# Performance work log

Measured on AMD Instinct MI355X. Metric: run time of the kernel, lower is better.

The kernel has to match this reference:

```python
import jax, jax.numpy as jnp
import numpy as np
from jax import lax

B, T, C = 2, 2048, 1024
HEAD = 64          # head_size N
H = C // HEAD      # n_head
EPS_GN = 0.00064   # GroupNorm epsilon from module


def l2norm(x, eps=1e-12):
    inv = lax.rsqrt(jnp.sum(x * x, axis=-1, keepdims=True) + eps)
    return x * jnp.maximum(inv, eps)


def group_norm(x, gamma, beta, groups, eps):
    n, c = x.shape
    xg = x.reshape(n, groups, c // groups)
    mu = jnp.mean(xg, axis=-1, keepdims=True)
    var = jnp.mean(jnp.square(xg - mu), axis=-1, keepdims=True)
    xg = (xg - mu) * lax.rsqrt(var + eps)
    return xg.reshape(n, c) * gamma + beta


def rwkv7_scan(r, w, k, v, a, b):
    # all [B,T,H,N]; w is log-decay, actual per-channel decay = exp(-exp(w))
    decay = jnp.exp(-jnp.exp(w))

    def step(state, inp):  # state: [B,H,N,N] (value dim i, key dim j)
        r_t, d_t, k_t, v_t, a_t, b_t = inp  # each [B,H,N]
        sa = jnp.einsum('bhij,bhj->bhi', state, a_t)
        state = (state * d_t[:, :, None, :]
                 + sa[:, :, :, None] * b_t[:, :, None, :]
                 + v_t[:, :, :, None] * k_t[:, :, None, :])
        out = jnp.einsum('bhij,bhj->bhi', state, r_t)
        return state, out

    xs = tuple(jnp.moveaxis(t, 1, 0) for t in (r, decay, k, v, a, b))
    state0 = jnp.zeros((r.shape[0], H, HEAD, HEAD), r.dtype)
    final_state, out = lax.scan(step, state0, xs)
    return jnp.moveaxis(out, 0, 1), final_state


def setup_inputs():
    key = jax.random.key(0)
    ks = jax.random.split(key, 32)

    def p(i, shape, scale=0.02):
        return jax.random.normal(ks[i], shape, jnp.float32) * scale

    return dict(
        x=jax.random.normal(ks[0], (B, T, C), jnp.float32),
        v_first=jax.random.normal(ks[1], (B, T, C), jnp.float32),
        x_r=p(2, (1, 1, C)), x_w=p(3, (1, 1, C)), x_k=p(4, (1, 1, C)),
        x_v=p(5, (1, 1, C)), x_a=p(6, (1, 1, C)), x_g=p(7, (1, 1, C)),
        w0=p(8, (1, 1, C)), w1=p(9, (C, 64)), w2=p(10, (64, C)),
        a0=p(11, (1, 1, C)), a1=p(12, (C, 64)), a2=p(13, (64, C)),
        v0=p(14, (1, 1, C)), v1=p(15, (C, 32)), v2=p(16, (32, C)),
        g1=p(17, (C, 128)), g2=p(18, (128, C)),
        k_k=p(19, (1, 1, C), 0.5), k_a=p(20, (1, 1, C), 0.5),
        r_k=p(21, (H, HEAD), 0.5),
        Wr=p(22, (C, C)), Wk=p(23, (C, C)), Wv=p(24, (C, C)), Wo=p(25, (C, C)),
        ln_gamma=jnp.ones((C,), jnp.float32),
        ln_beta=jnp.zeros((C,), jnp.float32),
    )


def reference(x, v_first, x_r, x_w, x_k, x_v, x_a, x_g, w0, w1, w2,
              a0, a1, a2, v0, v1, v2, g1, g2, k_k, k_a, r_k,
              Wr, Wk, Wv, Wo, ln_gamma, ln_beta):
    # time_shift(x) - x
    xx = jnp.pad(x, ((0, 0), (1, 0), (0, 0)))[:, :-1] - x
    xr = x + xx * x_r
    xw = x + xx * x_w
    xk = x + xx * x_k
    xv = x + xx * x_v
    xa = x + xx * x_a
    xg = x + xx * x_g

    r = xr @ Wr
    k = xk @ Wk
    v = xv @ Wv
    w = -jax.nn.softplus(-(w0 + jnp.tanh(xw @ w1) @ w2)) - 0.5
    # v_first provided (non-first layer path)
    v = v + (v_first - v) * jax.nn.sigmoid(v0 + (xv @ v1) @ v2)
    a = jax.nn.sigmoid(a0 + (xa @ a1) @ a2)
    g = jax.nn.sigmoid(xg @ g1) @ g2

    kk = l2norm((k * k_k).reshape(B, T, H, HEAD)).reshape(B, T, C)
    k = k * (1.0 + (a - 1.0) * k_a)

    r4 = r.reshape(B, T, H, HEAD)
    y, _ = rwkv7_scan(r4,
                      w.reshape(B, T, H, HEAD),
                      k.reshape(B, T, H, HEAD),
                      v.reshape(B, T, H, HEAD),
                      (-kk).reshape(B, T, H, HEAD),
                      (kk * a).reshape(B, T, H, HEAD))

    y = group_norm(y.reshape(B * T, C), ln_gamma, ln_beta, H, EPS_GN).reshape(B, T, C)

    k4 = k.reshape(B, T, H, HEAD)
    v4 = v.reshape(B, T, H, HEAD)
    rwkv = jnp.sum(r4 * k4 * r_k, axis=-1, keepdims=True) * v4  # [B,T,H,N]
    y = y + rwkv.reshape(B, T, C)
    return (y * g) @ Wo
```

## Files before the change

kernel.cpp:

```cpp
#include <hip/hip_runtime.h>
#include <hip/hip_bf16.h>
#include <math.h>

#define TSEQ 2048
#define HEADS 16
#define HSZ 64
#define CDIM 1024
#define MROWS 4096
#define CHUNK 64
#define NCHUNK (TSEQ/CHUNK)
#define NBH 32
#define LSTR 68
#define K2 2048

typedef short bf16x8 __attribute__((ext_vector_type(8)));
typedef short bf16x4 __attribute__((ext_vector_type(4)));
typedef float f32x4 __attribute__((ext_vector_type(4)));

__device__ __forceinline__ float sigf(float x) { return 1.0f / (1.0f + expf(-x)); }

__device__ __forceinline__ short to_bf16(float f) {
    __hip_bfloat16 h = __float2bfloat16(f);
    return *reinterpret_cast<short*>(&h);
}

__global__ __launch_bounds__(256)
void mix_make(const float* __restrict__ x, short* __restrict__ ax)
{
    const int m = blockIdx.x;
    const int cc = threadIdx.x * 4;
    const float4 xv = *(const float4*)(x + (size_t)m*CDIM + cc);
    float4 xp = make_float4(0.f, 0.f, 0.f, 0.f);
    if ((m & (TSEQ-1)) != 0) xp = *(const float4*)(x + (size_t)(m-1)*CDIM + cc);
    bf16x4 a, b;
    a[0] = to_bf16(xv.x); a[1] = to_bf16(xv.y);
    a[2] = to_bf16(xv.z); a[3] = to_bf16(xv.w);
    b[0] = to_bf16(xp.x - xv.x); b[1] = to_bf16(xp.y - xv.y);
    b[2] = to_bf16(xp.z - xv.z); b[3] = to_bf16(xp.w - xv.w);
    *(bf16x4*)(ax + (size_t)m*K2 + cc)        = a;
    *(bf16x4*)(ax + (size_t)m*K2 + CDIM + cc) = b;
}

__global__ __launch_bounds__(256)
void transpose_cvt(const float* __restrict__ W, short* __restrict__ Wt,
                   const int K, const int N)
{
    __shared__ float t[32][33];
    const int k0 = blockIdx.y * 32, n0 = blockIdx.x * 32;
    const int lx = threadIdx.x & 31, ly = threadIdx.x >> 5;
#pragma unroll
    for (int i = 0; i < 4; ++i)
        t[ly + i*8][lx] = W[(size_t)(k0 + ly + i*8)*N + n0 + lx];
    __syncthreads();
#pragma unroll
    for (int i = 0; i < 4; ++i)
        Wt[(size_t)(n0 + ly + i*8)*K + k0 + lx] = to_bf16(t[lx][ly + i*8]);
}

__global__ __launch_bounds__(256)
void transpose_cvt_scaled(const float* __restrict__ W, const float* __restrict__ mix,
                          short* __restrict__ Wt, const int N)
{
    __shared__ float t[32][33];
    const int k0 = blockIdx.y * 32, n0 = blockIdx.x * 32;
    const int lx = threadIdx.x & 31, ly = threadIdx.x >> 5;
#pragma unroll
    for (int i = 0; i < 4; ++i)
        t[ly + i*8][lx] = W[(size_t)(k0 + ly + i*8)*N + n0 + lx];
    __syncthreads();
    const float mv = mix[k0 + lx];
#pragma unroll
    for (int i = 0; i < 4; ++i) {
        const float w = t[lx][ly + i*8];
        short* base = Wt + (size_t)(n0 + ly + i*8)*K2 + k0 + lx;
        base[0]    = to_bf16(w);
        base[CDIM] = to_bf16(mv * w);
    }
}

template<int BN, int MODE>
__global__ __launch_bounds__(256)
void gemm_mfma(const short* __restrict__ A, const short* __restrict__ Bt,
               void* __restrict__ Cptr, const int M, const int N, const int K)
{
    constexpr int BM = 128, BK = 32;
    constexpr int ASTR = BK + 8;
    constexpr int NWC = (BN >= 128) ? 2 : 1;
    constexpr int NWR = 4 / NWC;
    constexpr int WM = BM / NWR;
    constexpr int WN = BN / NWC;
    constexpr int AM = WM / 16;
    constexpr int AN = WN / 16;

    __shared__ short As[BM * ASTR];
    __shared__ short Bs[BN * ASTR];

    const int tid  = threadIdx.x;
    const int bm   = blockIdx.y * BM;
    const int bn   = blockIdx.x * BN;
    const int wid  = tid >> 6;
    const int lane = tid & 63;
    const int wr   = wid / NWC;
    const int wc   = wid % NWC;
    const int lrow = lane & 15;
    const int koff = (lane >> 4) * 8;

    f32x4 acc[AM][AN];
#pragma unroll
    for (int m = 0; m < AM; ++m)
#pragma unroll
        for (int n = 0; n < AN; ++n)
            acc[m][n] = (f32x4){0.f, 0.f, 0.f, 0.f};

    for (int k0 = 0; k0 < K; k0 += BK) {
        __syncthreads();
#pragma unroll
        for (int p = 0; p < (BM*BK)/(256*8); ++p) {
            const int c = p*256 + tid;
            const int row = c >> 2;
            const int kc  = (c & 3) * 8;
            *(bf16x8*)&As[row*ASTR + kc] =
                *(const bf16x8*)(A + (size_t)(bm+row)*K + k0 + kc);
        }
        {
            constexpr int CHUNKS = (BN*BK)/8;
#pragma unroll
            for (int p = 0; p < (CHUNKS + 255)/256; ++p) {
                const int c = p*256 + tid;
                if ((CHUNKS & 255) == 0 || c < CHUNKS) {
                    const int col = c >> 2;
                    const int kc  = (c & 3) * 8;
                    *(bf16x8*)&Bs[col*ASTR + kc] =
                        *(const bf16x8*)(Bt + (size_t)(bn+col)*K + k0 + kc);
                }
            }
        }
        __syncthreads();

        bf16x8 af[AM], bfv[AN];
#pragma unroll
        for (int m = 0; m < AM; ++m)
            af[m] = *(const bf16x8*)&As[(wr*WM + m*16 + lrow)*ASTR + koff];
#pragma unroll
        for (int n = 0; n < AN; ++n)
            bfv[n] = *(const bf16x8*)&Bs[(wc*WN + n*16 + lrow)*ASTR + koff];
#pragma unroll
        for (int m = 0; m < AM; ++m)
#pragma unroll
            for (int n = 0; n < AN; ++n)
                acc[m][n] = __builtin_amdgcn_mfma_f32_16x16x32_bf16(
                    af[m], bfv[n], acc[m][n], 0, 0, 0);
    }

    const int r0 = (lane >> 4) * 4;
#pragma unroll
    for (int m = 0; m < AM; ++m) {
#pragma unroll
        for (int n = 0; n < AN; ++n) {
#pragma unroll
            for (int j = 0; j < 4; ++j) {
                const int row = bm + wr*WM + m*16 + r0 + j;
                const int col = bn + wc*WN + n*16 + lrow;
                float vv = acc[m][n][j];
                if (MODE == 0) {
                    ((float*)Cptr)[(size_t)row*N + col] = vv;
                } else if (MODE == 1) {
                    ((float*)Cptr)[(size_t)(col >> 10)*((size_t)MROWS*CDIM)
                                   + (size_t)row*CDIM + (col & 1023)] = vv;
                } else {
                    short* o = (short*)Cptr;
                    if (bn < 64)
                        o[(size_t)row*64 + col] = to_bf16(tanhf(vv));
                    else if (bn < 96)
                        (o + (size_t)MROWS*64)[(size_t)row*32 + col - 64] = to_bf16(vv);
                    else if (bn < 160)
                        (o + (size_t)MROWS*96)[(size_t)row*64 + col - 96] = to_bf16(vv);
                    else
                        (o + (size_t)MROWS*160)[(size_t)row*128 + col - 160] = to_bf16(sigf(vv));
                }
            }
        }
    }
}

__global__ __launch_bounds__(256)
void post_kernel(const float* __restrict__ tw, const float* __restrict__ vv,
                 const float* __restrict__ aa,
                 const float* __restrict__ w0, const float* __restrict__ v0p,
                 const float* __restrict__ a0p,
                 const float* __restrict__ k_k, const float* __restrict__ k_a,
                 const float* __restrict__ vfirst,
                 float* __restrict__ kio, float* __restrict__ vio,
                 float* __restrict__ dout, float* __restrict__ kkout,
                 float* __restrict__ bout)
{
    const int m  = blockIdx.x;
    const int c4 = threadIdx.x;
    const size_t o4 = (size_t)m*256 + c4;
    const int cc = c4*4;

    const float4 twv = ((const float4*)tw)[o4];
    const float4 vvv = ((const float4*)vv)[o4];
    const float4 aav = ((const float4*)aa)[o4];
    const float4 kv  = ((const float4*)kio)[o4];
    const float4 vv0 = ((const float4*)vio)[o4];
    const float4 vfv = ((const float4*)vfirst)[o4];
    const float4 w0v = *(const float4*)(w0 + cc);
    const float4 v0v = *(const float4*)(v0p + cc);
    const float4 a0v = *(const float4*)(a0p + cc);
    const float4 kkc = *(const float4*)(k_k + cc);
    const float4 kac = *(const float4*)(k_a + cc);

    float dec[4], vnew[4], av[4], kkr[4], knew[4];
    const float tws[4] = {twv.x, twv.y, twv.z, twv.w};
    const float vvs[4] = {vvv.x, vvv.y, vvv.z, vvv.w};
    const float aas[4] = {aav.x, aav.y, aav.z, aav.w};
    const float ks[4]  = {kv.x, kv.y, kv.z, kv.w};
    const float vs[4]  = {vv0.x, vv0.y, vv0.z, vv0.w};
    const float vfs[4] = {vfv.x, vfv.y, vfv.z, vfv.w};
    const float w0s[4] = {w0v.x, w0v.y, w0v.z, w0v.w};
    const float v0s[4] = {v0v.x, v0v.y, v0v.z, v0v.w};
    const float a0s[4] = {a0v.x, a0v.y, a0v.z, a0v.w};
    const float kks[4] = {kkc.x, kkc.y, kkc.z, kkc.w};
    const float kas[4] = {kac.x, kac.y, kac.z, kac.w};

    float ss = 0.f;
#pragma unroll
    for (int i = 0; i < 4; ++i) {
        dec[i]  = expf(-0.6065306597126334f * sigf(w0s[i] + tws[i]));
        const float sv = sigf(v0s[i] + vvs[i]);
        vnew[i] = vs[i] + (vfs[i] - vs[i]) * sv;
        av[i]   = sigf(a0s[i] + aas[i]);
        kkr[i]  = ks[i] * kks[i];
        knew[i] = ks[i] * (1.f + (av[i] - 1.f) * kas[i]);
        ss = fmaf(kkr[i], kkr[i], ss);
    }
#pragma unroll
    for (int mask = 1; mask < 16; mask <<= 1) ss += __shfl_xor(ss, mask);
    const float inv = fmaxf(rsqrtf(ss + 1e-12f), 1e-12f);

    float4 decv, vnv, knv, kkv4, bv4;
    decv.x = dec[0]; decv.y = dec[1]; decv.z = dec[2]; decv.w = dec[3];
    vnv.x = vnew[0]; vnv.y = vnew[1]; vnv.z = vnew[2]; vnv.w = vnew[3];
    knv.x = knew[0]; knv.y = knew[1]; knv.z = knew[2]; knv.w = knew[3];
    kkv4.x = kkr[0]*inv; kkv4.y = kkr[1]*inv; kkv4.z = kkr[2]*inv; kkv4.w = kkr[3]*inv;
    bv4.x = kkv4.x*av[0]; bv4.y = kkv4.y*av[1]; bv4.z = kkv4.z*av[2]; bv4.w = kkv4.w*av[3];

    ((float4*)dout)[o4]  = decv;
    ((float4*)vio)[o4]   = vnv;
    ((float4*)kio)[o4]   = knv;
    ((float4*)kkout)[o4] = kkv4;
    ((float4*)bout)[o4]  = bv4;
}

__global__ __launch_bounds__(128)
void scan_pass1(const float* __restrict__ d, const float* __restrict__ k,
                const float* __restrict__ v, const float* __restrict__ kk,
                const float* __restrict__ bb,
                float* __restrict__ Gbuf, float* __restrict__ Hbuf)
{
    const int chunk = blockIdx.x;
    const int bh = blockIdx.y;
    const int b = bh >> 4, h = bh & 15;
    const int tid = threadIdx.x;
    const int lane = tid & 63;
    const int isH = tid >> 6;

    __shared__ float sv[4][64];

    float row[HSZ];
#pragma unroll
    for (int j = 0; j < HSZ; ++j)
        row[j] = (!isH && j == lane) ? 1.f : 0.f;

    size_t off = ((size_t)b*TSEQ + (size_t)chunk*CHUNK) * CDIM + h*HSZ;
    for (int t = 0; t < CHUNK; ++t, off += CDIM) {
        const float vi = isH ? v[off + lane] : 0.f;
        __syncthreads();
        if (!isH) { sv[0][lane] = kk[off + lane]; sv[2][lane] = bb[off + lane]; }
        else      { sv[1][lane] = d[off + lane];  sv[3][lane] = k[off + lane]; }
        __syncthreads();

        float g0 = 0.f, g1 = 0.f, g2 = 0.f, g3 = 0.f;
#pragma unroll
        for (int j4 = 0; j4 < 16; ++j4) {
            const float4 kv = *(const float4*)&sv[0][j4*4];
            g0 = fmaf(row[j4*4+0], kv.x, g0);
            g1 = fmaf(row[j4*4+1], kv.y, g1);
            g2 = fmaf(row[j4*4+2], kv.z, g2);
            g3 = fmaf(row[j4*4+3], kv.w, g3);
        }
        const float ga = -((g0 + g1) + (g2 + g3));

        if (isH) {
#pragma unroll
            for (int j4 = 0; j4 < 16; ++j4) {
                const float4 dv = *(const float4*)&sv[1][j4*4];
                const float4 bv = *(const float4*)&sv[2][j4*4];
                const float4 kv = *(const float4*)&sv[3][j4*4];
                row[j4*4+0] = fmaf(row[j4*4+0], dv.x, fmaf(ga, bv.x, vi * kv.x));
                row[j4*4+1] = fmaf(row[j4*4+1], dv.y, fmaf(ga, bv.y, vi * kv.y));
                row[j4*4+2] = fmaf(row[j4*4+2], dv.z, fmaf(ga, bv.z, vi * kv.z));
                row[j4*4+3] = fmaf(row[j4*4+3], dv.w, fmaf(ga, bv.w, vi * kv.w));
            }
        } else {
#pragma unroll
            for (int j4 = 0; j4 < 16; ++j4) {
                const float4 dv = *(const float4*)&sv[1][j4*4];
                const float4 bv = *(const float4*)&sv[2][j4*4];
                row[j4*4+0] = fmaf(row[j4*4+0], dv.x, ga * bv.x);
                row[j4*4+1] = fmaf(row[j4*4+1], dv.y, ga * bv.y);
                row[j4*4+2] = fmaf(row[j4*4+2], dv.z, ga * bv.z);
                row[j4*4+3] = fmaf(row[j4*4+3], dv.w, ga * bv.w);
            }
        }
    }

    float* dst = (isH ? Hbuf : Gbuf) + (((size_t)bh*NCHUNK + chunk)*HSZ + lane)*HSZ;
#pragma unroll
    for (int j4 = 0; j4 < 16; ++j4)
        *(float4*)&dst[j4*4] = make_float4(row[j4*4+0], row[j4*4+1], row[j4*4+2], row[j4*4+3]);
}

__global__ __launch_bounds__(256)
void scan_pass2(const float* __restrict__ Gbuf, const float* __restrict__ Hbuf,
                float* __restrict__ S0buf)
{
    const int rg = blockIdx.x;
    const int bh = blockIdx.y;
    const int tid = threadIdx.x;
    const int il = tid & 15;
    const int q4 = tid >> 4;
    const int row = rg*16 + il;

    __shared__ float Gs[64][68];
    __shared__ float Ssh[16][68];

    float frag[4] = {0.f, 0.f, 0.f, 0.f};
    *(float4*)&Ssh[il][q4*4] = make_float4(0.f, 0.f, 0.f, 0.f);

    for (int c = 0; c < NCHUNK; ++c) {
        const size_t mbase = ((size_t)bh*NCHUNK + c)*HSZ*HSZ;
#pragma unroll
        for (int p = 0; p < 4; ++p) {
            const int f = tid*16 + p*4;
            const int rr = f >> 6, cc = f & 63;
            *(float4*)&Gs[rr][cc] = *(const float4*)(Gbuf + mbase + f);
        }
        *(float4*)(S0buf + mbase + (size_t)row*HSZ + q4*4) =
            make_float4(frag[0], frag[1], frag[2], frag[3]);
        __syncthreads();

        float4 hv = *(const float4*)(Hbuf + mbase + (size_t)row*HSZ + q4*4);
        float a0 = hv.x, a1 = hv.y, a2 = hv.z, a3 = hv.w;
#pragma unroll
        for (int j = 0; j < 64; ++j) {
            const float sj = Ssh[il][j];
            const float4 gv = *(const float4*)&Gs[j][q4*4];
            a0 = fmaf(sj, gv.x, a0);
            a1 = fmaf(sj, gv.y, a1);
            a2 = fmaf(sj, gv.z, a2);
            a3 = fmaf(sj, gv.w, a3);
        }
        __syncthreads();
        frag[0] = a0; frag[1] = a1; frag[2] = a2; frag[3] = a3;
        *(float4*)&Ssh[il][q4*4] = make_float4(a0, a1, a2, a3);
    }
}

__device__ __forceinline__ void zero44(f32x4 a[4][4]) {
#pragma unroll
    for (int m = 0; m < 4; ++m)
#pragma unroll
        for (int n = 0; n < 4; ++n) a[m][n] = (f32x4){0.f, 0.f, 0.f, 0.f};
}

__device__ __forceinline__ void mm_nt_lds(const short* __restrict__ Ab,
                                          const short* __restrict__ Bb,
                                          f32x4 acc[4][4], const int lane)
{
    const int lrow = lane & 15;
    const int ko   = (lane >> 4) * 8;
#pragma unroll
    for (int kh = 0; kh < 2; ++kh) {
        bf16x8 af[4], bfv[4];
#pragma unroll
        for (int m = 0; m < 4; ++m)
            af[m] = *(const bf16x8*)&Ab[(m*16 + lrow)*LSTR + kh*32 + ko];
#pragma unroll
        for (int n = 0; n < 4; ++n)
            bfv[n] = *(const bf16x8*)&Bb[(n*16 + lrow)*LSTR + kh*32 + ko];
#pragma unroll
        for (int m = 0; m < 4; ++m)
#pragma unroll
            for (int n = 0; n < 4; ++n)
                acc[m][n] = __builtin_amdgcn_mfma_f32_16x16x32_bf16(
                    af[m], bfv[n], acc[m][n], 0, 0, 0);
    }
}

__device__ __forceinline__ void mm_nt_gf32(const short* __restrict__ Ab,
                                           const float* __restrict__ Bg,
                                           f32x4 acc[4][4], const int lane)
{
    const int lrow = lane & 15;
    const int ko   = (lane >> 4) * 8;
#pragma unroll
    for (int kh = 0; kh < 2; ++kh) {
        bf16x8 af[4], bfv[4];
#pragma unroll
        for (int m = 0; m < 4; ++m)
            af[m] = *(const bf16x8*)&Ab[(m*16 + lrow)*LSTR + kh*32 + ko];
#pragma unroll
        for (int n = 0; n < 4; ++n) {
            const float* p = Bg + (size_t)(n*16 + lrow)*64 + kh*32 + ko;
            const float4 u0 = *(const float4*)p;
            const float4 u1 = *(const float4*)(p + 4);
            bf16x8 bv;
            bv[0] = to_bf16(u0.x); bv[1] = to_bf16(u0.y);
            bv[2] = to_bf16(u0.z); bv[3] = to_bf16(u0.w);
            bv[4] = to_bf16(u1.x); bv[5] = to_bf16(u1.y);
            bv[6] = to_bf16(u1.z); bv[7] = to_bf16(u1.w);
            bfv[n] = bv;
        }
#pragma unroll
        for (int m = 0; m < 4; ++m)
#pragma unroll
            for (int n = 0; n < 4; ++n)
                acc[m][n] = __builtin_amdgcn_mfma_f32_16x16x32_bf16(
                    af[m], bfv[n], acc[m][n], 0, 0, 0);
    }
}

template<int MASK, bool WRN, bool WRT>
__device__ __forceinline__ void acc_store(const f32x4 acc[4][4],
                                          short* __restrict__ dst,
                                          short* __restrict__ dstT,
                                          const int lane)
{
    const int r0 = (lane >> 4) * 4;
    const int c0 = lane & 15;
#pragma unroll
    for (int m = 0; m < 4; ++m)
#pragma unroll
        for (int n = 0; n < 4; ++n)
#pragma unroll
            for (int j = 0; j < 4; ++j) {
                const int row = m*16 + r0 + j;
                const int col = n*16 + c0;
                float vv = acc[m][n][j];
                if (MASK == 1 && col >= row) vv = 0.f;
                if (MASK == 2 && col >  row) vv = 0.f;
                const short bv = to_bf16(vv);
                if (WRN) dst [row*LSTR + col] = bv;
                if (WRT) dstT[col*LSTR + row] = bv;
            }
}

__global__ __launch_bounds__(64)
void scan_pass3_mfma(const float* __restrict__ r, const float* __restrict__ d,
                     const float* __restrict__ k, const float* __restrict__ v,
                     const float* __restrict__ kk, const float* __restrict__ bb,
                     const float* __restrict__ S0buf, float* __restrict__ y)
{
    __shared__ short Ah[64*LSTR], Bh[64*LSTR], Kh[64*LSTR], Rh[64*LSTR];
    __shared__ short Vt[64*LSTR], Cb[64*LSTR], Nb[64*LSTR], Nt[64*LSTR], Xt[64*LSTR];

    const int chunk = blockIdx.x;
    const int bh = blockIdx.y;
    const int b = bh >> 4, h = bh & 15;
    const int lane = threadIdx.x;

    size_t off = ((size_t)b*TSEQ + (size_t)chunk*CHUNK)*CDIM + h*HSZ + lane;
    float run = 0.f;
    for (int t = 0; t < CHUNK; ++t, off += CDIM) {
        const float de    = d[off];
        const float cprev = run;
        run += logf(de);
        Ah[t*LSTR + lane] = to_bf16(-kk[off] * expf(cprev));
        Bh[t*LSTR + lane] = to_bf16(bb[off] * expf(-run));
        Kh[t*LSTR + lane] = to_bf16(k[off]  * expf(-run));
        Rh[t*LSTR + lane] = to_bf16(r[off]  * expf(run));
        Vt[lane*LSTR + t] = to_bf16(v[off]);
    }
    __syncthreads();

    const float* S0g = S0buf + ((size_t)bh*NCHUNK + chunk)*HSZ*HSZ;

    f32x4 acc[4][4], xacc[4][4];

    zero44(acc);  mm_nt_lds(Ah, Bh, acc, lane);
    acc_store<1, true, true>(acc, Nb, Nt, lane);
    zero44(acc);  mm_nt_lds(Ah, Kh, acc, lane);
    acc_store<1, true, false>(acc, Cb, nullptr, lane);
    __syncthreads();

    zero44(xacc);
    mm_nt_gf32(Ah, S0g, xacc, lane);
    mm_nt_lds(Cb, Vt, xacc, lane);
    acc_store<0, false, true>(xacc, nullptr, Xt, lane);
    __syncthreads();

#pragma unroll 1
    for (int rd = 0; rd < 6; ++rd) {
        mm_nt_lds(Nb, Xt, xacc, lane);
        if (rd < 5) { zero44(acc); mm_nt_lds(Nb, Nt, acc, lane); }
        __syncthreads();
        acc_store<0, false, true>(xacc, nullptr, Xt, lane);
        if (rd < 5) acc_store<0, true, true>(acc, Nb, Nt, lane);
        __syncthreads();
    }

    zero44(acc);  mm_nt_lds(Rh, Bh, acc, lane);
    acc_store<2, true, false>(acc, Cb, nullptr, lane);
    zero44(acc);  mm_nt_lds(Rh, Kh, acc, lane);
    acc_store<2, true, false>(acc, Nb, nullptr, lane);
    __syncthreads();

    zero44(acc);
    mm_nt_gf32(Rh, S0g, acc, lane);
    mm_nt_lds(Cb, Xt, acc, lane);
    mm_nt_lds(Nb, Vt, acc, lane);

    const int r0 = (lane >> 4) * 4;
    const int c0 = lane & 15;
    float* yb = y + ((size_t)b*TSEQ + (size_t)chunk*CHUNK)*CDIM + h*HSZ;
#pragma unroll
    for (int m = 0; m < 4; ++m)
#pragma unroll
        for (int n = 0; n < 4; ++n)
#pragma unroll
            for (int j = 0; j < 4; ++j)
                yb[(size_t)(m*16 + r0 + j)*CDIM + n*16 + c0] = acc[m][n][j];
}

__global__ __launch_bounds__(1024)
void gn_kernel(const float* __restrict__ r, const float* __restrict__ k,
               const float* __restrict__ v, const float* __restrict__ g,
               const float* __restrict__ rk, const float* __restrict__ gamma,
               const float* __restrict__ beta, const float* __restrict__ y,
               short* __restrict__ ybf)
{
    const int m = blockIdx.x;
    const int c = threadIdx.x;
    const size_t o = (size_t)m*CDIM + c;
    const float yv = y[o];
    float s1 = yv, s2 = yv*yv;
#pragma unroll
    for (int mask = 1; mask < 64; mask <<= 1) {
        s1 += __shfl_xor(s1, mask);
        s2 += __shfl_xor(s2, mask);
    }
    const float mu  = s1 * (1.f/HSZ);
    const float var = s2 * (1.f/HSZ) - mu*mu;
    const float gn  = (yv - mu) * rsqrtf(var + 0.00064f) * gamma[c] + beta[c];

    float p = r[o] * k[o] * rk[c];
#pragma unroll
    for (int mask = 1; mask < 64; mask <<= 1) p += __shfl_xor(p, mask);

    ybf[o] = to_bf16((gn + p * v[o]) * g[o]);
}

extern "C" void kernel_launch(void* const* d_in, const int* in_sizes, int n_in,
                              void* d_out, int out_size, void* d_ws, size_t ws_size,
                              hipStream_t stream)
{
    const float* x      = (const float*)d_in[0];
    const float* vfirst = (const float*)d_in[1];
    const float* x_r = (const float*)d_in[2];
    const float* x_w = (const float*)d_in[3];
    const float* x_k = (const float*)d_in[4];
    const float* x_v = (const float*)d_in[5];
    const float* x_a = (const float*)d_in[6];
    const float* x_g = (const float*)d_in[7];
    const float* w0  = (const float*)d_in[8];
    const float* w1  = (const float*)d_in[9];
    const float* w2  = (const float*)d_in[10];
    const float* a0  = (const float*)d_in[11];
    const float* a1  = (const float*)d_in[12];
    const float* a2  = (const float*)d_in[13];
    const float* v0p = (const float*)d_in[14];
    const float* v1  = (const float*)d_in[15];
    const float* v2  = (const float*)d_in[16];
    const float* g1  = (const float*)d_in[17];
    const float* g2  = (const float*)d_in[18];
    const float* k_k = (const float*)d_in[19];
    const float* k_a = (const float*)d_in[20];
    const float* r_k = (const float*)d_in[21];
    const float* Wr  = (const float*)d_in[22];
    const float* Wk  = (const float*)d_in[23];
    const float* Wv  = (const float*)d_in[24];
    const float* Wo  = (const float*)d_in[25];
    const float* lng = (const float*)d_in[26];
    const float* lnb = (const float*)d_in[27];
    float* outp = (float*)d_out;

    float* ws = (float*)d_ws;
    const size_t BIG = (size_t)MROWS * CDIM;
    float* rbuf  = ws + 0*BIG;
    float* kbuf  = ws + 1*BIG;
    float* vbuf  = ws + 2*BIG;
    float* dbuf  = ws + 3*BIG;
    float* kkbuf = ws + 4*BIG;
    float* bbuf  = ws + 5*BIG;
    float* gbuf  = ws + 6*BIG;
    float* ybuf  = ws + 7*BIG;
    float* smbuf = ws + 8*BIG;
    short* hwbf  = (short*)smbuf;
    short* wT    = (short*)(smbuf + (size_t)MROWS*160/2);
    short* Brkv = wT;
    short* Bsm  = Brkv + (size_t)3072*K2;
    short* WoT  = Bsm  + (size_t)288*K2;
    short* g2T  = WoT  + (size_t)CDIM*CDIM;
    short* w2T  = g2T  + (size_t)CDIM*128;
    short* v2T  = w2T  + (size_t)CDIM*64;
    short* a2T  = v2T  + (size_t)CDIM*32;
    short* axbf = a2T  + (size_t)CDIM*64;

    float* twbuf = ybuf;
    float* vvbuf = gbuf;
    float* aabuf = outp;

    float* Gbuf  = ybuf;
    float* Hbuf  = gbuf;
    float* S0buf = outp;
    short* ybf   = (short*)dbuf;
    short* ghbf  = hwbf + (size_t)MROWS*160;

    const dim3 blk(256);

    mix_make<<<dim3(MROWS), blk, 0, stream>>>(x, axbf);
    transpose_cvt_scaled<<<dim3(CDIM/32, CDIM/32), blk, 0, stream>>>(Wr, x_r, Brkv, CDIM);
    transpose_cvt_scaled<<<dim3(CDIM/32, CDIM/32), blk, 0, stream>>>(Wk, x_k, Brkv + (size_t)1024*K2, CDIM);
    transpose_cvt_scaled<<<dim3(CDIM/32, CDIM/32), blk, 0, stream>>>(Wv, x_v, Brkv + (size_t)2048*K2, CDIM);
    transpose_cvt_scaled<<<dim3(64/32,   CDIM/32), blk, 0, stream>>>(w1, x_w, Bsm, 64);
    transpose_cvt_scaled<<<dim3(32/32,   CDIM/32), blk, 0, stream>>>(v1, x_v, Bsm + (size_t)64*K2, 32);
    transpose_cvt_scaled<<<dim3(64/32,   CDIM/32), blk, 0, stream>>>(a1, x_a, Bsm + (size_t)96*K2, 64);
    transpose_cvt_scaled<<<dim3(128/32,  CDIM/32), blk, 0, stream>>>(g1, x_g, Bsm + (size_t)160*K2, 128);
    transpose_cvt<<<dim3(CDIM/32, CDIM/32), blk, 0, stream>>>(Wo, WoT, CDIM, CDIM);
    transpose_cvt<<<dim3(CDIM/32, 128/32),  blk, 0, stream>>>(g2, g2T, 128, CDIM);
    transpose_cvt<<<dim3(CDIM/32, 64/32),   blk, 0, stream>>>(w2, w2T, 64, CDIM);
    transpose_cvt<<<dim3(CDIM/32, 32/32),   blk, 0, stream>>>(v2, v2T, 32, CDIM);
    transpose_cvt<<<dim3(CDIM/32, 64/32),   blk, 0, stream>>>(a2, a2T, 64, CDIM);

    gemm_mfma<128,1><<<dim3(3072/128, MROWS/128), blk, 0, stream>>>(
        axbf, Brkv, rbuf, MROWS, 3072, K2);
    gemm_mfma<32,2><<<dim3(288/32, MROWS/128), blk, 0, stream>>>(
        axbf, Bsm, hwbf, MROWS, 288, K2);
    gemm_mfma<128,0><<<dim3(CDIM/128, MROWS/128), blk, 0, stream>>>(
        hwbf, w2T, twbuf, MROWS, CDIM, 64);
    gemm_mfma<128,0><<<dim3(CDIM/128, MROWS/128), blk, 0, stream>>>(
        hwbf + (size_t)MROWS*64, v2T, vvbuf, MROWS, CDIM, 32);
    gemm_mfma<128,0><<<dim3(CDIM/128, MROWS/128), blk, 0, stream>>>(
        hwbf + (size_t)MROWS*96, a2T, aabuf, MROWS, CDIM, 64);

    post_kernel<<<dim3(MROWS), blk, 0, stream>>>(
        twbuf, vvbuf, aabuf, w0, v0p, a0, k_k, k_a, vfirst,
        kbuf, vbuf, dbuf, kkbuf, bbuf);

    scan_pass1<<<dim3(NCHUNK, NBH), dim3(128), 0, stream>>>(
        dbuf, kbuf, vbuf, kkbuf, bbuf, Gbuf, Hbuf);
    scan_pass2<<<dim3(4, NBH), dim3(256), 0, stream>>>(Gbuf, Hbuf, S0buf);
    scan_pass3_mfma<<<dim3(NCHUNK, NBH), dim3(64), 0, stream>>>(
        rbuf, dbuf, kbuf, vbuf, kkbuf, bbuf, S0buf, ybuf);

    gemm_mfma<128,0><<<dim3(CDIM/128, MROWS/128), blk, 0, stream>>>(
        ghbf, g2T, gbuf, MROWS, CDIM, 128);

    gn_kernel<<<dim3(MROWS), dim3(1024), 0, stream>>>(
        rbuf, kbuf, vbuf, gbuf, r_k, lng, lnb, ybuf, ybf);

    gemm_mfma<128,0><<<dim3(CDIM/128, MROWS/128), blk, 0, stream>>>(
        ybf, WoT, outp, MROWS, CDIM, CDIM);
}
```

Measured before the change: 492.6 us.

## Replace sequential chunk-transition scan with WY-form MFMA pass and lighter output pass

The per-chunk transition matrices G and H are now built with MFMA matrix products in a WY-style factorisation, using the inverted triangular system from the doubling iterations. The old pass built them with a 64-step sequential recurrence on scalar FMAs. The WY factors Y and U are stored in bf16 so the third pass skips recomputing the triangular inverse and only applies them with the carried-in state. Both chunk kernels now use four waves per block, each owning 16 rows, instead of one or two waves. This adds bf16 rounding in G/H and the stored factors and reuses the axbf buffer as scratch, which may hurt accuracy.

```diff
diff --git a/kernel.cpp b/kernel.cpp
--- a/kernel.cpp
+++ b/kernel.cpp
@@ -22,6 +22,10 @@
 __device__ __forceinline__ short to_bf16(float f) {
     __hip_bfloat16 h = __float2bfloat16(f);
     return *reinterpret_cast<short*>(&h);
+}
+__device__ __forceinline__ float bf2f(short s) {
+    unsigned int u = ((unsigned int)(unsigned short)s) << 16;
+    return __uint_as_float(u);
 }
 
 __global__ __launch_bounds__(256)
@@ -253,164 +257,39 @@
     ((float4*)bout)[o4]  = bv4;
 }
 
-__global__ __launch_bounds__(128)
-void scan_pass1(const float* __restrict__ d, const float* __restrict__ k,
-                const float* __restrict__ v, const float* __restrict__ kk,
-                const float* __restrict__ bb,
-                float* __restrict__ Gbuf, float* __restrict__ Hbuf)
-{
-    const int chunk = blockIdx.x;
-    const int bh = blockIdx.y;
-    const int b = bh >> 4, h = bh & 15;
-    const int tid = threadIdx.x;
-    const int lane = tid & 63;
-    const int isH = tid >> 6;
-
-    __shared__ float sv[4][64];
-
-    float row[HSZ];
-#pragma unroll
-    for (int j = 0; j < HSZ; ++j)
-        row[j] = (!isH && j == lane) ? 1.f : 0.f;
-
-    size_t off = ((size_t)b*TSEQ + (size_t)chunk*CHUNK) * CDIM + h*HSZ;
-    for (int t = 0; t < CHUNK; ++t, off += CDIM) {
-        const float vi = isH ? v[off + lane] : 0.f;
-        __syncthreads();
-        if (!isH) { sv[0][lane] = kk[off + lane]; sv[2][lane] = bb[off + lane]; }
-        else      { sv[1][lane] = d[off + lane];  sv[3][lane] = k[off + lane]; }
-        __syncthreads();
-
-        float g0 = 0.f, g1 = 0.f, g2 = 0.f, g3 = 0.f;
-#pragma unroll
-        for (int j4 = 0; j4 < 16; ++j4) {
-            const float4 kv = *(const float4*)&sv[0][j4*4];
-            g0 = fmaf(row[j4*4+0], kv.x, g0);
-            g1 = fmaf(row[j4*4+1], kv.y, g1);
-            g2 = fmaf(row[j4*4+2], kv.z, g2);
-            g3 = fmaf(row[j4*4+3], kv.w, g3);
-        }
-        const float ga = -((g0 + g1) + (g2 + g3));
-
-        if (isH) {
-#pragma unroll
-            for (int j4 = 0; j4 < 16; ++j4) {
-                const float4 dv = *(const float4*)&sv[1][j4*4];
-                const float4 bv = *(const float4*)&sv[2][j4*4];
-                const float4 kv = *(const float4*)&sv[3][j4*4];
-                row[j4*4+0] = fmaf(row[j4*4+0], dv.x, fmaf(ga, bv.x, vi * kv.x));
-                row[j4*4+1] = fmaf(row[j4*4+1], dv.y, fmaf(ga, bv.y, vi * kv.y));
-                row[j4*4+2] = fmaf(row[j4*4+2], dv.z, fmaf(ga, bv.z, vi * kv.z));
-                row[j4*4+3] = fmaf(row[j4*4+3], dv.w, fmaf(ga, bv.w, vi * kv.w));
-            }
-        } else {
-#pragma unroll
-            for (int j4 = 0; j4 < 16; ++j4) {
-                const float4 dv = *(const float4*)&sv[1][j4*4];
-                const float4 bv = *(const float4*)&sv[2][j4*4];
-                row[j4*4+0] = fmaf(row[j4*4+0], dv.x, ga * bv.x);
-                row[j4*4+1] = fmaf(row[j4*4+1], dv.y, ga * bv.y);
-                row[j4*4+2] = fmaf(row[j4*4+2], dv.z, ga * bv.z);
-                row[j4*4+3] = fmaf(row[j4*4+3], dv.w, ga * bv.w);
-            }
-        }
-    }
-
-    float* dst = (isH ? Hbuf : Gbuf) + (((size_t)bh*NCHUNK + chunk)*HSZ + lane)*HSZ;
-#pragma unroll
-    for (int j4 = 0; j4 < 16; ++j4)
-        *(float4*)&dst[j4*4] = make_float4(row[j4*4+0], row[j4*4+1], row[j4*4+2], row[j4*4+3]);
-}
-
-__global__ __launch_bounds__(256)
-void scan_pass2(const float* __restrict__ Gbuf, const float* __restrict__ Hbuf,
-                float* __restrict__ S0buf)
-{
-    const int rg = blockIdx.x;
-    const int bh = blockIdx.y;
-    const int tid = threadIdx.x;
-    const int il = tid & 15;
-    const int q4 = tid >> 4;
-    const int row = rg*16 + il;
-
-    __shared__ float Gs[64][68];
-    __shared__ float Ssh[16][68];
-
-    float frag[4] = {0.f, 0.f, 0.f, 0.f};
-    *(float4*)&Ssh[il][q4*4] = make_float4(0.f, 0.f, 0.f, 0.f);
-
-    for (int c = 0; c < NCHUNK; ++c) {
-        const size_t mbase = ((size_t)bh*NCHUNK + c)*HSZ*HSZ;
-#pragma unroll
-        for (int p = 0; p < 4; ++p) {
-            const int f = tid*16 + p*4;
-            const int rr = f >> 6, cc = f & 63;
-            *(float4*)&Gs[rr][cc] = *(const float4*)(Gbuf + mbase + f);
-        }
-        *(float4*)(S0buf + mbase + (size_t)row*HSZ + q4*4) =
-            make_float4(frag[0], frag[1], frag[2], frag[3]);
-        __syncthreads();
-
-        float4 hv = *(const float4*)(Hbuf + mbase + (size_t)row*HSZ + q4*4);
-        float a0 = hv.x, a1 = hv.y, a2 = hv.z, a3 = hv.w;
-#pragma unroll
-        for (int j = 0; j < 64; ++j) {
-            const float sj = Ssh[il][j];
-            const float4 gv = *(const float4*)&Gs[j][q4*4];
-            a0 = fmaf(sj, gv.x, a0);
-            a1 = fmaf(sj, gv.y, a1);
-            a2 = fmaf(sj, gv.z, a2);
-            a3 = fmaf(sj, gv.w, a3);
-        }
-        __syncthreads();
-        frag[0] = a0; frag[1] = a1; frag[2] = a2; frag[3] = a3;
-        *(float4*)&Ssh[il][q4*4] = make_float4(a0, a1, a2, a3);
-    }
-}
-
-__device__ __forceinline__ void zero44(f32x4 a[4][4]) {
-#pragma unroll
-    for (int m = 0; m < 4; ++m)
-#pragma unroll
-        for (int n = 0; n < 4; ++n) a[m][n] = (f32x4){0.f, 0.f, 0.f, 0.f};
-}
-
-__device__ __forceinline__ void mm_nt_lds(const short* __restrict__ Ab,
-                                          const short* __restrict__ Bb,
-                                          f32x4 acc[4][4], const int lane)
+__device__ __forceinline__ void zero4(f32x4 a[4]) {
+#pragma unroll
+    for (int n = 0; n < 4; ++n) a[n] = (f32x4){0.f, 0.f, 0.f, 0.f};
+}
+
+__device__ __forceinline__ void mm_nt_w(const short* __restrict__ Ab,
+                                        const short* __restrict__ Bb,
+                                        f32x4 acc[4], const int lane, const int woff)
 {
     const int lrow = lane & 15;
     const int ko   = (lane >> 4) * 8;
 #pragma unroll
     for (int kh = 0; kh < 2; ++kh) {
-        bf16x8 af[4], bfv[4];
-#pragma unroll
-        for (int m = 0; m < 4; ++m)
-            af[m] = *(const bf16x8*)&Ab[(m*16 + lrow)*LSTR + kh*32 + ko];
+        const bf16x8 af = *(const bf16x8*)&Ab[(woff + lrow)*LSTR + kh*32 + ko];
+        bf16x8 bv[4];
 #pragma unroll
         for (int n = 0; n < 4; ++n)
-            bfv[n] = *(const bf16x8*)&Bb[(n*16 + lrow)*LSTR + kh*32 + ko];
-#pragma unroll
-        for (int m = 0; m < 4; ++m)
-#pragma unroll
-            for (int n = 0; n < 4; ++n)
-                acc[m][n] = __builtin_amdgcn_mfma_f32_16x16x32_bf16(
-                    af[m], bfv[n], acc[m][n], 0, 0, 0);
-    }
-}
-
-__device__ __forceinline__ void mm_nt_gf32(const short* __restrict__ Ab,
-                                           const float* __restrict__ Bg,
-                                           f32x4 acc[4][4], const int lane)
+            bv[n] = *(const bf16x8*)&Bb[(n*16 + lrow)*LSTR + kh*32 + ko];
+#pragma unroll
+        for (int n = 0; n < 4; ++n)
+            acc[n] = __builtin_amdgcn_mfma_f32_16x16x32_bf16(af, bv[n], acc[n], 0, 0, 0);
+    }
+}
+
+__device__ __forceinline__ void mm_nt_gf32_w(const short* __restrict__ Ab,
+                                             const float* __restrict__ Bg,
+                                             f32x4 acc[4], const int lane, const int woff)
 {
     const int lrow = lane & 15;
     const int ko   = (lane >> 4) * 8;
 #pragma unroll
     for (int kh = 0; kh < 2; ++kh) {
-        bf16x8 af[4], bfv[4];
-#pragma unroll
-        for (int m = 0; m < 4; ++m)
-            af[m] = *(const bf16x8*)&Ab[(m*16 + lrow)*LSTR + kh*32 + ko];
+        const bf16x8 af = *(const bf16x8*)&Ab[(woff + lrow)*LSTR + kh*32 + ko];
 #pragma unroll
         for (int n = 0; n < 4; ++n) {
             const float* p = Bg + (size_t)(n*16 + lrow)*64 + kh*32 + ko;
@@ -421,117 +300,316 @@
             bv[2] = to_bf16(u0.z); bv[3] = to_bf16(u0.w);
             bv[4] = to_bf16(u1.x); bv[5] = to_bf16(u1.y);
             bv[6] = to_bf16(u1.z); bv[7] = to_bf16(u1.w);
-            bfv[n] = bv;
-        }
-#pragma unroll
-        for (int m = 0; m < 4; ++m)
-#pragma unroll
-            for (int n = 0; n < 4; ++n)
-                acc[m][n] = __builtin_amdgcn_mfma_f32_16x16x32_bf16(
-                    af[m], bfv[n], acc[m][n], 0, 0, 0);
+            acc[n] = __builtin_amdgcn_mfma_f32_16x16x32_bf16(af, bv, acc[n], 0, 0, 0);
+        }
     }
 }
 
 template<int MASK, bool WRN, bool WRT>
-__device__ __forceinline__ void acc_store(const f32x4 acc[4][4],
-                                          short* __restrict__ dst,
-                                          short* __restrict__ dstT,
-                                          const int lane)
+__device__ __forceinline__ void acc_store_w(const f32x4 acc[4],
+                                            short* __restrict__ dst,
+                                            short* __restrict__ dstT,
+                                            const int lane, const int woff)
 {
     const int r0 = (lane >> 4) * 4;
     const int c0 = lane & 15;
 #pragma unroll
-    for (int m = 0; m < 4; ++m)
-#pragma unroll
-        for (int n = 0; n < 4; ++n)
-#pragma unroll
-            for (int j = 0; j < 4; ++j) {
-                const int row = m*16 + r0 + j;
-                const int col = n*16 + c0;
-                float vv = acc[m][n][j];
-                if (MASK == 1 && col >= row) vv = 0.f;
-                if (MASK == 2 && col >  row) vv = 0.f;
-                const short bv = to_bf16(vv);
-                if (WRN) dst [row*LSTR + col] = bv;
-                if (WRT) dstT[col*LSTR + row] = bv;
-            }
-}
-
-__global__ __launch_bounds__(64)
-void scan_pass3_mfma(const float* __restrict__ r, const float* __restrict__ d,
-                     const float* __restrict__ k, const float* __restrict__ v,
-                     const float* __restrict__ kk, const float* __restrict__ bb,
-                     const float* __restrict__ S0buf, float* __restrict__ y)
-{
-    __shared__ short Ah[64*LSTR], Bh[64*LSTR], Kh[64*LSTR], Rh[64*LSTR];
-    __shared__ short Vt[64*LSTR], Cb[64*LSTR], Nb[64*LSTR], Nt[64*LSTR], Xt[64*LSTR];
+    for (int n = 0; n < 4; ++n)
+#pragma unroll
+        for (int j = 0; j < 4; ++j) {
+            const int row = woff + r0 + j;
+            const int col = n*16 + c0;
+            float vv = acc[n][j];
+            if (MASK == 1 && col >= row) vv = 0.f;
+            if (MASK == 2 && col >  row) vv = 0.f;
+            const short bv = to_bf16(vv);
+            if (WRN) dst [row*LSTR + col] = bv;
+            if (WRT) dstT[col*LSTR + row] = bv;
+        }
+}
+
+__device__ __forceinline__ void acc_init_lds_w(f32x4 acc[4],
+                                               const short* __restrict__ src,
+                                               const int lane, const int woff)
+{
+    const int r0 = (lane >> 4) * 4;
+    const int c0 = lane & 15;
+#pragma unroll
+    for (int n = 0; n < 4; ++n)
+#pragma unroll
+        for (int j = 0; j < 4; ++j)
+            acc[n][j] = bf2f(src[(woff + r0 + j)*LSTR + n*16 + c0]);
+}
+
+__device__ __forceinline__ void acc_init_glb_w(f32x4 acc[4],
+                                               const short* __restrict__ src,
+                                               const int lane, const int woff)
+{
+    const int r0 = (lane >> 4) * 4;
+    const int c0 = lane & 15;
+#pragma unroll
+    for (int n = 0; n < 4; ++n)
+#pragma unroll
+        for (int j = 0; j < 4; ++j)
+            acc[n][j] = bf2f(src[(woff + r0 + j)*64 + n*16 + c0]);
+}
+
+__global__ __launch_bounds__(256)
+void scan_pass1_wy(const float* __restrict__ d, const float* __restrict__ k,
+                   const float* __restrict__ v, const float* __restrict__ kk,
+                   const float* __restrict__ bb,
+                   float* __restrict__ Gbuf, float* __restrict__ Hbuf,
+                   short* __restrict__ Yg, short* __restrict__ Ug)
+{
+    __shared__ short L[8*64*LSTR];
+    __shared__ float wsum[4][64];
+    __shared__ float cTl[64];
+    short* A_  = L + 0*64*LSTR;
+    short* B_  = L + 1*64*LSTR;
+    short* K_  = L + 2*64*LSTR;
+    short* V_  = L + 3*64*LSTR;
+    short* BT_ = L + 4*64*LSTR;
+    short* KT_ = L + 5*64*LSTR;
+    short* N_  = L + 6*64*LSTR;
+    short* NT_ = L + 7*64*LSTR;
 
     const int chunk = blockIdx.x;
     const int bh = blockIdx.y;
     const int b = bh >> 4, h = bh & 15;
-    const int lane = threadIdx.x;
-
-    size_t off = ((size_t)b*TSEQ + (size_t)chunk*CHUNK)*CDIM + h*HSZ + lane;
-    float run = 0.f;
-    for (int t = 0; t < CHUNK; ++t, off += CDIM) {
-        const float de    = d[off];
-        const float cprev = run;
-        run += logf(de);
-        Ah[t*LSTR + lane] = to_bf16(-kk[off] * expf(cprev));
-        Bh[t*LSTR + lane] = to_bf16(bb[off] * expf(-run));
-        Kh[t*LSTR + lane] = to_bf16(k[off]  * expf(-run));
-        Rh[t*LSTR + lane] = to_bf16(r[off]  * expf(run));
-        Vt[lane*LSTR + t] = to_bf16(v[off]);
-    }
-    __syncthreads();
-
-    const float* S0g = S0buf + ((size_t)bh*NCHUNK + chunk)*HSZ*HSZ;
-
-    f32x4 acc[4][4], xacc[4][4];
-
-    zero44(acc);  mm_nt_lds(Ah, Bh, acc, lane);
-    acc_store<1, true, true>(acc, Nb, Nt, lane);
-    zero44(acc);  mm_nt_lds(Ah, Kh, acc, lane);
-    acc_store<1, true, false>(acc, Cb, nullptr, lane);
-    __syncthreads();
-
-    zero44(xacc);
-    mm_nt_gf32(Ah, S0g, xacc, lane);
-    mm_nt_lds(Cb, Vt, xacc, lane);
-    acc_store<0, false, true>(xacc, nullptr, Xt, lane);
+    const int tid = threadIdx.x;
+    const int w = tid >> 6;
+    const int lane = tid & 63;
+    const int woff = w * 16;
+
+    const size_t base = ((size_t)b*TSEQ + (size_t)chunk*CHUNK + woff)*CDIM + h*HSZ + lane;
+    float lc[16];
+    float s = 0.f;
+#pragma unroll
+    for (int t = 0; t < 16; ++t) { s += logf(d[base + (size_t)t*CDIM]); lc[t] = s; }
+    wsum[w][lane] = s;
+    __syncthreads();
+    float pre = 0.f;
+#pragma unroll
+    for (int w2 = 0; w2 < 3; ++w2) if (w2 < w) pre += wsum[w2][lane];
+    if (w == 3) cTl[lane] = expf(pre + s);
+
+#pragma unroll
+    for (int t = 0; t < 16; ++t) {
+        const int tg = woff + t;
+        const size_t off = base + (size_t)t*CDIM;
+        const float run   = pre + lc[t];
+        const float cprev = (t == 0) ? pre : (pre + lc[t-1]);
+        const float ern   = expf(-run);
+        A_[tg*LSTR + lane] = to_bf16(-kk[off] * expf(cprev));
+        const short bv = to_bf16(bb[off] * ern);
+        B_[tg*LSTR + lane] = bv;  BT_[lane*LSTR + tg] = bv;
+        const short kv = to_bf16(k[off] * ern);
+        K_[tg*LSTR + lane] = kv;  KT_[lane*LSTR + tg] = kv;
+        V_[lane*LSTR + tg] = to_bf16(v[off]);
+    }
+    __syncthreads();
+
+    f32x4 xj[4], xi[4], tmp[4];
+
+    zero4(tmp);  mm_nt_w(A_, B_, tmp, lane, woff);
+    acc_init_lds_w(xj, A_, lane, woff);
+    acc_store_w<1, true, true>(tmp, N_, NT_, lane, woff);
+    __syncthreads();
+
+    acc_store_w<0, false, true>(xj, nullptr, B_, lane, woff);
+    zero4(tmp);  mm_nt_w(A_, K_, tmp, lane, woff);
+    __syncthreads();
+    acc_store_w<1, true, false>(tmp, K_, nullptr, lane, woff);
+    __syncthreads();
+
+    zero4(xi);  mm_nt_w(K_, V_, xi, lane, woff);
+    acc_store_w<0, false, true>(xi, nullptr, A_, lane, woff);
     __syncthreads();
 
 #pragma unroll 1
     for (int rd = 0; rd < 6; ++rd) {
-        mm_nt_lds(Nb, Xt, xacc, lane);
-        if (rd < 5) { zero44(acc); mm_nt_lds(Nb, Nt, acc, lane); }
+        mm_nt_w(N_, B_, xj, lane, woff);
+        mm_nt_w(N_, A_, xi, lane, woff);
+        if (rd < 5) { zero4(tmp); mm_nt_w(N_, NT_, tmp, lane, woff); }
         __syncthreads();
-        acc_store<0, false, true>(xacc, nullptr, Xt, lane);
-        if (rd < 5) acc_store<0, true, true>(acc, Nb, Nt, lane);
+        acc_store_w<0, false, true>(xj, nullptr, B_, lane, woff);
+        acc_store_w<0, false, true>(xi, nullptr, A_, lane, woff);
+        if (rd < 5) acc_store_w<0, true, true>(tmp, N_, NT_, lane, woff);
         __syncthreads();
     }
 
-    zero44(acc);  mm_nt_lds(Rh, Bh, acc, lane);
-    acc_store<2, true, false>(acc, Cb, nullptr, lane);
-    zero44(acc);  mm_nt_lds(Rh, Kh, acc, lane);
-    acc_store<2, true, false>(acc, Nb, nullptr, lane);
-    __syncthreads();
-
-    zero44(acc);
-    mm_nt_gf32(Rh, S0g, acc, lane);
-    mm_nt_lds(Cb, Xt, acc, lane);
-    mm_nt_lds(Nb, Vt, acc, lane);
+    const size_t mb = ((size_t)bh*NCHUNK + chunk)*HSZ*HSZ;
+    const int r0 = (lane >> 4) * 4;
+    const int c0 = lane & 15;
+
+#pragma unroll
+    for (int n = 0; n < 4; ++n)
+#pragma unroll
+        for (int j = 0; j < 4; ++j) {
+            const int row = woff + r0 + j;
+            const int col = n*16 + c0;
+            Yg[mb + row*64 + col] = to_bf16(xj[n][j]);
+            Ug[mb + row*64 + col] = to_bf16(xi[n][j]);
+        }
+
+    float ctv[4];
+#pragma unroll
+    for (int n = 0; n < 4; ++n) ctv[n] = cTl[n*16 + c0];
+
+    zero4(tmp);  mm_nt_w(B_, BT_, tmp, lane, woff);
+#pragma unroll
+    for (int n = 0; n < 4; ++n)
+#pragma unroll
+        for (int j = 0; j < 4; ++j) {
+            const int row = woff + r0 + j;
+            const int col = n*16 + c0;
+            const float id = (row == col) ? 1.f : 0.f;
+            Gbuf[mb + (size_t)row*HSZ + col] = (tmp[n][j] + id) * ctv[n];
+        }
+
+    zero4(tmp);
+    mm_nt_w(A_, BT_, tmp, lane, woff);
+    mm_nt_w(V_, KT_, tmp, lane, woff);
+#pragma unroll
+    for (int n = 0; n < 4; ++n)
+#pragma unroll
+        for (int j = 0; j < 4; ++j) {
+            const int row = woff + r0 + j;
+            const int col = n*16 + c0;
+            Hbuf[mb + (size_t)row*HSZ + col] = tmp[n][j] * ctv[n];
+        }
+}
+
+__global__ __launch_bounds__(256)
+void scan_pass2(const float* __restrict__ Gbuf, const float* __restrict__ Hbuf,
+                float* __restrict__ S0buf)
+{
+    const int rg = blockIdx.x;
+    const int bh = blockIdx.y;
+    const int tid = threadIdx.x;
+    const int il = tid & 15;
+    const int q4 = tid >> 4;
+    const int row = rg*16 + il;
+
+    __shared__ float Gs[64][68];
+    __shared__ float Ssh[16][68];
+
+    float frag[4] = {0.f, 0.f, 0.f, 0.f};
+    *(float4*)&Ssh[il][q4*4] = make_float4(0.f, 0.f, 0.f, 0.f);
+
+    for (int c = 0; c < NCHUNK; ++c) {
+        const size_t mbase = ((size_t)bh*NCHUNK + c)*HSZ*HSZ;
+#pragma unroll
+        for (int p = 0; p < 4; ++p) {
+            const int f = tid*16 + p*4;
+            const int rr = f >> 6, cc = f & 63;
+            *(float4*)&Gs[rr][cc] = *(const float4*)(Gbuf + mbase + f);
+        }
+        *(float4*)(S0buf + mbase + (size_t)row*HSZ + q4*4) =
+            make_float4(frag[0], frag[1], frag[2], frag[3]);
+        __syncthreads();
+
+        float4 hv = *(const float4*)(Hbuf + mbase + (size_t)row*HSZ + q4*4);
+        float a0 = hv.x, a1 = hv.y, a2 = hv.z, a3 = hv.w;
+#pragma unroll
+        for (int j = 0; j < 64; ++j) {
+            const float sj = Ssh[il][j];
+            const float4 gv = *(const float4*)&Gs[j][q4*4];
+            a0 = fmaf(sj, gv.x, a0);
+            a1 = fmaf(sj, gv.y, a1);
+            a2 = fmaf(sj, gv.z, a2);
+            a3 = fmaf(sj, gv.w, a3);
+        }
+        __syncthreads();
+        frag[0] = a0; frag[1] = a1; frag[2] = a2; frag[3] = a3;
+        *(float4*)&Ssh[il][q4*4] = make_float4(a0, a1, a2, a3);
+    }
+}
+
+__global__ __launch_bounds__(256)
+void scan_pass3_lite4(const float* __restrict__ r, const float* __restrict__ d,
+                      const float* __restrict__ k, const float* __restrict__ v,
+                      const float* __restrict__ bb,
+                      const short* __restrict__ Yg, const short* __restrict__ Ug,
+                      const float* __restrict__ S0buf, float* __restrict__ y)
+{
+    __shared__ short L[8*64*LSTR];
+    __shared__ float wsum[4][64];
+    short* R_  = L + 0*64*LSTR;
+    short* B_  = L + 1*64*LSTR;
+    short* K_  = L + 2*64*LSTR;
+    short* V_  = L + 3*64*LSTR;
+    short* Yn  = L + 4*64*LSTR;
+    short* Wt  = L + 5*64*LSTR;
+    short* P1b = L + 6*64*LSTR;
+    short* P2b = L + 7*64*LSTR;
+
+    const int chunk = blockIdx.x;
+    const int bh = blockIdx.y;
+    const int b = bh >> 4, h = bh & 15;
+    const int tid = threadIdx.x;
+    const int w = tid >> 6;
+    const int lane = tid & 63;
+    const int woff = w * 16;
+    const size_t mb = ((size_t)bh*NCHUNK + chunk)*HSZ*HSZ;
+
+    const size_t base = ((size_t)b*TSEQ + (size_t)chunk*CHUNK + woff)*CDIM + h*HSZ + lane;
+    float lc[16];
+    float s = 0.f;
+#pragma unroll
+    for (int t = 0; t < 16; ++t) { s += logf(d[base + (size_t)t*CDIM]); lc[t] = s; }
+    wsum[w][lane] = s;
+    __syncthreads();
+    float pre = 0.f;
+#pragma unroll
+    for (int w2 = 0; w2 < 3; ++w2) if (w2 < w) pre += wsum[w2][lane];
+
+#pragma unroll
+    for (int t = 0; t < 16; ++t) {
+        const int tg = woff + t;
+        const size_t off = base + (size_t)t*CDIM;
+        const float run = pre + lc[t];
+        const float ern = expf(-run);
+        R_[tg*LSTR + lane] = to_bf16(r[off] * expf(run));
+        B_[tg*LSTR + lane] = to_bf16(bb[off] * ern);
+        K_[tg*LSTR + lane] = to_bf16(k[off]  * ern);
+        V_[lane*LSTR + tg] = to_bf16(v[off]);
+    }
+    {
+        const int row = woff + (lane & 15);
+        const int cb  = (lane >> 4) * 16;
+        const short* yp = Yg + mb + (size_t)row*64 + cb;
+        *(bf16x8*)&Yn[row*LSTR + cb]     = *(const bf16x8*)yp;
+        *(bf16x8*)&Yn[row*LSTR + cb + 8] = *(const bf16x8*)(yp + 8);
+    }
+    __syncthreads();
+
+    const float* S0g = S0buf + mb;
+    f32x4 a4[4], o4[4];
+
+    acc_init_glb_w(a4, Ug + mb, lane, woff);
+    mm_nt_gf32_w(Yn, S0g, a4, lane, woff);
+    acc_store_w<0, false, true>(a4, nullptr, Wt, lane, woff);
+
+    zero4(a4);  mm_nt_w(R_, B_, a4, lane, woff);
+    acc_store_w<2, true, false>(a4, P1b, nullptr, lane, woff);
+    zero4(a4);  mm_nt_w(R_, K_, a4, lane, woff);
+    acc_store_w<2, true, false>(a4, P2b, nullptr, lane, woff);
+    __syncthreads();
+
+    zero4(o4);
+    mm_nt_gf32_w(R_, S0g, o4, lane, woff);
+    mm_nt_w(P1b, Wt, o4, lane, woff);
+    mm_nt_w(P2b, V_, o4, lane, woff);
 
     const int r0 = (lane >> 4) * 4;
     const int c0 = lane & 15;
     float* yb = y + ((size_t)b*TSEQ + (size_t)chunk*CHUNK)*CDIM + h*HSZ;
 #pragma unroll
-    for (int m = 0; m < 4; ++m)
-#pragma unroll
-        for (int n = 0; n < 4; ++n)
-#pragma unroll
-            for (int j = 0; j < 4; ++j)
-                yb[(size_t)(m*16 + r0 + j)*CDIM + n*16 + c0] = acc[m][n][j];
+    for (int n = 0; n < 4; ++n)
+#pragma unroll
+        for (int j = 0; j < 4; ++j)
+            yb[(size_t)(woff + r0 + j)*CDIM + n*16 + c0] = o4[n][j];
 }
 
 __global__ __launch_bounds__(1024)
@@ -618,6 +696,9 @@
     short* a2T  = v2T  + (size_t)CDIM*32;
     short* axbf = a2T  + (size_t)CDIM*64;
 
+    short* Yg = axbf;
+    short* Ug = axbf + (size_t)NBH*NCHUNK*HSZ*HSZ;
+
     float* twbuf = ybuf;
     float* vvbuf = gbuf;
     float* aabuf = outp;
@@ -659,11 +740,11 @@
         twbuf, vvbuf, aabuf, w0, v0p, a0, k_k, k_a, vfirst,
         kbuf, vbuf, dbuf, kkbuf, bbuf);
 
-    scan_pass1<<<dim3(NCHUNK, NBH), dim3(128), 0, stream>>>(
-        dbuf, kbuf, vbuf, kkbuf, bbuf, Gbuf, Hbuf);
-    scan_pass2<<<dim3(4, NBH), dim3(256), 0, stream>>>(Gbuf, Hbuf, S0buf);
-    scan_pass3_mfma<<<dim3(NCHUNK, NBH), dim3(64), 0, stream>>>(
-        rbuf, dbuf, kbuf, vbuf, kkbuf, bbuf, S0buf, ybuf);
+    scan_pass1_wy<<<dim3(NCHUNK, NBH), blk, 0, stream>>>(
+        dbuf, kbuf, vbuf, kkbuf, bbuf, Gbuf, Hbuf, Yg, Ug);
+    scan_pass2<<<dim3(4, NBH), blk, 0, stream>>>(Gbuf, Hbuf, S0buf);
+    scan_pass3_lite4<<<dim3(NCHUNK, NBH), blk, 0, stream>>>(
+        rbuf, dbuf, kbuf, vbuf, bbuf, Yg, Ug, S0buf, ybuf);
 
     gemm_mfma<128,0><<<dim3(CDIM/128, MROWS/128), blk, 0, stream>>>(
         ghbf, g2T, gbuf, MROWS, CDIM, 128);
```

Measured after the change: 469.0 us. 1.05x faster.
